# Kernel optimization log

Hardware: AMD Instinct MI355X
Metric: run time of the kernel (lower is better)

Reference implementation:

```python
import jax, jax.numpy as jnp
import numpy as np

GRAN = 4      # mask_spatial_granularity
STRIDE = 1    # dilate_stride
PAD = 1       # ExpandMask padding -> 3x3 all-ones dilation kernel


def setup_inputs() -> dict:
    key = jax.random.key(0)
    k1, k2, k3 = jax.random.split(key, 3)
    B, C, H, W = 32, 64, 112, 112
    G = 4
    mh, mw = H // STRIDE // GRAN, W // STRIDE // GRAN
    x = jax.random.normal(k1, (B, C, H, W), jnp.float32)
    weight = jax.random.normal(k2, (2 * G, C), jnp.float32) * 0.05  # 1x1 conv
    bias = jnp.zeros((2 * G,), jnp.float32).at[:G].set(5.0).at[G + 1:].set(1.0)
    # standard gumbel(0,1) noise for gumbel_softmax
    u = jax.random.uniform(k3, (B, 2, G, mh, mw), jnp.float32, 1e-10, 1.0)
    gumbel = -jnp.log(-jnp.log(u))
    temperature = jnp.float32(1.0)
    return {"x": x, "weight": weight, "bias": bias, "gumbel": gumbel,
            "temperature": temperature}


def reference(x, weight, bias, gumbel, temperature):
    B, C, H, W = x.shape
    G = weight.shape[0] // 2
    mh, mw = H // STRIDE // GRAN, W // STRIDE // GRAN   # mask grid (28,28)
    fh, fw = H // STRIDE, W // STRIDE                   # feature size (112,112)

    # adaptive_avg_pool2d (H,W evenly divisible by mask grid)
    m = x.reshape(B, C, mh, H // mh, mw, W // mw).mean(axis=(3, 5))
    flops = C * mh * mw
    # 1x1 conv
    m = jnp.einsum('bchw,oc->bohw', m, weight) + bias[None, :, None, None]
    flops += (weight.shape[0] * weight.shape[1] + weight.shape[1]) * mh * mw

    # gumbel_softmax over dim=1 with hard=True (straight-through)
    logits = m.reshape(B, 2, G, mh, mw)
    y_soft = jax.nn.softmax((logits + gumbel) / temperature, axis=1)
    idx = jnp.argmax(y_soft, axis=1)
    y_hard = jax.nn.one_hot(idx, 2, axis=1, dtype=y_soft.dtype)
    y = y_hard - jax.lax.stop_gradient(y_soft) + y_soft
    mask = y[:, 0]                                      # [B,G,mh,mw]
    sparsity = mask.sum() / mask.size

    # F.interpolate(size=feature_size), default mode='nearest' with integer factor
    mask = jnp.repeat(jnp.repeat(mask, fh // mh, axis=2), fw // mw, axis=3)

    # ExpandMask (stride=1): 3x3 all-ones full (cross-channel) conv, then >0.5
    dk = jnp.ones((G, G, 1 + 2 * PAD, 1 + 2 * PAD), mask.dtype)
    dil = jax.lax.conv_general_dilated(
        mask, dk, window_strides=(1, 1), padding=((PAD, PAD), (PAD, PAD)),
        dimension_numbers=('NCHW', 'OIHW', 'NCHW'))
    mask_dil = dil > 0.5
    sparsity_dil = jnp.mean(mask_dil.astype(jnp.float32))

    return mask, mask_dil, sparsity, sparsity_dil, flops
```

## Files before the change

kernel.cpp:

```cpp
#include <hip/hip_runtime.h>

#define MH 28
#define MW 28
#define CC 64
#define GG 4
#define NB 32
#define RPB 2

typedef float vf4 __attribute__((ext_vector_type(4)));

__device__ __forceinline__ int xcd_swz896(int phys) {
    return (phys & 7) * 112 + (phys >> 3);
}
__device__ __forceinline__ int xcd_swz448(int phys) {
    return (phys & 7) * 56 + (phys >> 3);
}


__global__ __launch_bounds__(256, 3) void masker_d1(
    const float* __restrict__ x, const float* __restrict__ w,
    const float* __restrict__ bias, const float* __restrict__ gum,
    unsigned char* __restrict__ coarse, unsigned char* __restrict__ anyb)
{
    const int blk = xcd_swz448(blockIdx.x);
    const int b = blk / 14, rp = blk - (blk / 14) * 14;
    const int chA = 2 * rp, chB = 2 * rp + 1;
    const int t = threadIdx.x;

    __shared__ float pooled[RPB][CC][MW];
    __shared__ float wlds[8 * CC];
    __shared__ float logits[RPB][8][MW];
    __shared__ unsigned char mlds[RPB][GG][MW];

    float g0a = 0.f, g1a = 0.f, g0b = 0.f, g1b = 0.f, bo = 0.f;
    if (t < GG * MW) {
        int g = t / MW, cw = t - g * MW;
        g0a = gum[((((size_t)b * 2 + 0) * GG + g) * MH + chA) * MW + cw];
        g1a = gum[((((size_t)b * 2 + 1) * GG + g) * MH + chA) * MW + cw];
        g0b = gum[((((size_t)b * 2 + 0) * GG + g) * MH + chB) * MW + cw];
        g1b = gum[((((size_t)b * 2 + 1) * GG + g) * MH + chB) * MW + cw];
    }
    if (t < 8 * MW) bo = bias[t / MW];
    if (t < 128) ((float4*)wlds)[t] = ((const float4*)w)[t];

    const float* xb = x + (size_t)b * CC * 12544 + (size_t)(8 * rp) * 112;
    #pragma unroll
    for (int r = 0; r < RPB; ++r) {
        vf4 rr[7][4];
        #pragma unroll
        for (int k = 0; k < 7; ++k) {
            int p  = t + 256 * k;
            int c  = p / MW;
            int cw = p - c * MW;
            const vf4* base = (const vf4*)(xb + (size_t)c * 12544
                                              + (size_t)(4 * r) * 112 + 4 * cw);
            #pragma unroll
            for (int hh = 0; hh < 4; ++hh)
                rr[k][hh] = __builtin_nontemporal_load(base + hh * 28);
        }
        #pragma unroll
        for (int k = 0; k < 7; ++k) {
            int p  = t + 256 * k;
            int c  = p / MW;
            int cw = p - c * MW;
            float s = 0.f;
            #pragma unroll
            for (int hh = 0; hh < 4; ++hh)
                s += rr[k][hh].x + rr[k][hh].y + rr[k][hh].z + rr[k][hh].w;
            pooled[r][c][cw] = s * 0.0625f;
        }
    }
    __syncthreads();

    if (t < 8 * MW) {
        int o = t / MW, cw = t - o * MW;
        float accA = bo, accB = bo;
        #pragma unroll
        for (int c = 0; c < CC; ++c) {
            float wv = wlds[o * CC + c];
            accA += pooled[0][c][cw] * wv;
            accB += pooled[1][c][cw] * wv;
        }
        logits[0][o][cw] = accA;
        logits[1][o][cw] = accB;
    }
    __syncthreads();

    if (t < GG * MW) {
        int g = t / MW, cw = t - g * MW;
        unsigned char mvA = (logits[0][g][cw] + g0a >= logits[0][g + 4][cw] + g1a) ? 1u : 0u;
        unsigned char mvB = (logits[1][g][cw] + g0b >= logits[1][g + 4][cw] + g1b) ? 1u : 0u;
        mlds[0][g][cw] = mvA;
        mlds[1][g][cw] = mvB;
        coarse[(((size_t)b * GG + g) * MH + chA) * MW + cw] = mvA;
        coarse[(((size_t)b * GG + g) * MH + chB) * MW + cw] = mvB;
    }
    __syncthreads();
    if (t < 2 * MW) {
        int r = t / MW, cw = t - r * MW;
        unsigned char a = mlds[r][0][cw] | mlds[r][1][cw] | mlds[r][2][cw] | mlds[r][3][cw];
        anyb[((size_t)b * MH + (2 * rp + r)) * MW + cw] = a;
    }
}

__global__ __launch_bounds__(256) void masker_d2(
    const unsigned char* __restrict__ coarse,
    const unsigned char* __restrict__ anyb,
    float* __restrict__ out_mask, float* __restrict__ out_dil,
    uint2* __restrict__ slots)
{
    const int blk = xcd_swz896(blockIdx.x);
    int b = blk / MH, ch = blk - (blk / MH) * MH, t = threadIdx.x;
    __shared__ float carr[GG][MW];
    __shared__ float R[3][MW + 2];
    __shared__ unsigned int sm[4], sd[4];

    unsigned int local_m = 0;
    if (t < GG * MW) {
        int g = t / MW, cw = t - g * MW;
        unsigned char mv = coarse[(((size_t)b * GG + g) * MH + ch) * MW + cw];
        carr[g][cw] = (float)mv;
        local_m = mv;
    }
    if (t < MW) {
        float a  = (float)anyb[((size_t)b * MH + ch) * MW + t];
        float am = (ch > 0)      ? (float)anyb[((size_t)b * MH + ch - 1) * MW + t] : 0.f;
        float ap = (ch < MH - 1) ? (float)anyb[((size_t)b * MH + ch + 1) * MW + t] : 0.f;
        R[0][t + 1] = fmaxf(a, am);
        R[1][t + 1] = a;
        R[2][t + 1] = fmaxf(a, ap);
    }
    if (t < 3) { R[t][0] = 0.f; R[t][MW + 1] = 0.f; }
    __syncthreads();

    unsigned int local_d = 0;
    #pragma unroll
    for (int k = 0; k < 7; ++k) {
        int idx = t + 256 * k;
        int g   = idx / 448;
        int rem = idx - g * 448;
        int hh  = rem / 112;
        int wfi = rem - hh * 112;
        int cw  = wfi >> 2;
        int wm  = wfi & 3;
        int rv  = (hh == 0) ? 0 : (hh == 3 ? 2 : 1);
        float d;
        if (wm == 0)      d = fmaxf(R[rv][cw],     R[rv][cw + 1]);
        else if (wm == 3) d = fmaxf(R[rv][cw + 1], R[rv][cw + 2]);
        else              d = R[rv][cw + 1];
        float mv = carr[g][cw];
        size_t o = (((size_t)b * GG + g) * 112 + (4 * ch + hh)) * 112 + wfi;
        __builtin_nontemporal_store(mv, &out_mask[o]);
        __builtin_nontemporal_store(d,  &out_dil[o]);
        local_d += (d > 0.5f) ? 1u : 0u;
    }

    #pragma unroll
    for (int off = 32; off; off >>= 1) {
        local_m += __shfl_down(local_m, off);
        local_d += __shfl_down(local_d, off);
    }
    if ((t & 63) == 0) { sm[t >> 6] = local_m; sd[t >> 6] = local_d; }
    __syncthreads();
    if (t == 0) {
        uint2 v;
        v.x = sm[0] + sm[1] + sm[2] + sm[3];
        v.y = sd[0] + sd[1] + sd[2] + sd[3];
        slots[blk] = v;
    }
}

__global__ __launch_bounds__(256) void masker_d3(
    const uint2* __restrict__ slots, float* __restrict__ out_scalars)
{
    int t = threadIdx.x;
    unsigned int m = 0, d = 0;
    for (int i = t; i < NB * MH; i += 256) { uint2 v = slots[i]; m += v.x; d += v.y; }
    #pragma unroll
    for (int off = 32; off; off >>= 1) {
        m += __shfl_down(m, off);
        d += __shfl_down(d, off);
    }
    __shared__ unsigned int sm[4], sd[4];
    if ((t & 63) == 0) { sm[t >> 6] = m; sd[t >> 6] = d; }
    __syncthreads();
    if (t == 0) {
        out_scalars[0] = (float)(sm[0] + sm[1] + sm[2] + sm[3]) / 100352.0f;
        out_scalars[1] = (float)(sd[0] + sd[1] + sd[2] + sd[3]) / 1605632.0f;
        out_scalars[2] = 501760.0f;
    }
}

extern "C" void kernel_launch(void* const* d_in, const int* in_sizes, int n_in,
                              void* d_out, int out_size, void* d_ws, size_t ws_size,
                              hipStream_t stream) {
    const float* x    = (const float*)d_in[0];
    const float* w    = (const float*)d_in[1];
    const float* bias = (const float*)d_in[2];
    const float* gum  = (const float*)d_in[3];

    float* out = (float*)d_out;
    const size_t n_mask = (size_t)NB * GG * 112 * 112;

    uint2*         slots  = (uint2*)d_ws;
    unsigned char* coarse = (unsigned char*)d_ws + 8192;
    unsigned char* anyb   = (unsigned char*)d_ws + 8192 + 100352;

    masker_d1<<<dim3(NB * MH / RPB), 256, 0, stream>>>(x, w, bias, gum, coarse, anyb);
    masker_d2<<<dim3(NB * MH), 256, 0, stream>>>(coarse, anyb, out, out + n_mask, slots);
    masker_d3<<<1, 256, 0, stream>>>(slots, out + 2 * n_mask);
}
```

Baseline: 28.00 us.

## Load contiguous channel slabs and pool via LDS row sums

The pooling phase now loads each channel's contiguous 8-row slab with consecutive threads covering consecutive float4s, instead of strided per-pooling-window loads. Each float4 is reduced to a row sum in a 28 KB shared buffer, and a second pass combines four row sums per pooled cell. The goal is fully coalesced global reads with more loads in flight per thread (28 float4). The cost is higher register pressure, more LDS use (which may reduce occupancy under launch_bounds 3) and extra barriers.

```diff
diff --git a/kernel.cpp b/kernel.cpp
--- a/kernel.cpp
+++ b/kernel.cpp
@@ -9,12 +9,8 @@
 
 typedef float vf4 __attribute__((ext_vector_type(4)));
 
-__device__ __forceinline__ int xcd_swz896(int phys) {
-    return (phys & 7) * 112 + (phys >> 3);
-}
-__device__ __forceinline__ int xcd_swz448(int phys) {
-    return (phys & 7) * 56 + (phys >> 3);
-}
+__device__ __forceinline__ int xcd_swz896(int phys) { return (phys & 7) * 112 + (phys >> 3); }
+__device__ __forceinline__ int xcd_swz448(int phys) { return (phys & 7) * 56  + (phys >> 3); }
 
 
 __global__ __launch_bounds__(256, 3) void masker_d1(
@@ -27,6 +23,7 @@
     const int chA = 2 * rp, chB = 2 * rp + 1;
     const int t = threadIdx.x;
 
+    __shared__ float rowsum[32 * 8 * MW];
     __shared__ float pooled[RPB][CC][MW];
     __shared__ float wlds[8 * CC];
     __shared__ float logits[RPB][8][MW];
@@ -44,33 +41,37 @@
     if (t < 128) ((float4*)wlds)[t] = ((const float4*)w)[t];
 
     const float* xb = x + (size_t)b * CC * 12544 + (size_t)(8 * rp) * 112;
-    #pragma unroll
-    for (int r = 0; r < RPB; ++r) {
-        vf4 rr[7][4];
+
+    #pragma unroll
+    for (int h = 0; h < 2; ++h) {
+        vf4 r[28];
+        #pragma unroll
+        for (int j = 0; j < 28; ++j) {
+            int f = t + 256 * j;
+            int s = f / 224;
+            int off = f - s * 224;
+            r[j] = __builtin_nontemporal_load(
+                (const vf4*)(xb + (size_t)(h * 32 + s) * 12544) + off);
+        }
+        #pragma unroll
+        for (int j = 0; j < 28; ++j) {
+            int f = t + 256 * j;
+            rowsum[f] = r[j].x + r[j].y + r[j].z + r[j].w;
+        }
+        __syncthreads();
         #pragma unroll
         for (int k = 0; k < 7; ++k) {
-            int p  = t + 256 * k;
-            int c  = p / MW;
-            int cw = p - c * MW;
-            const vf4* base = (const vf4*)(xb + (size_t)c * 12544
-                                              + (size_t)(4 * r) * 112 + 4 * cw);
-            #pragma unroll
-            for (int hh = 0; hh < 4; ++hh)
-                rr[k][hh] = __builtin_nontemporal_load(base + hh * 28);
-        }
-        #pragma unroll
-        for (int k = 0; k < 7; ++k) {
-            int p  = t + 256 * k;
-            int c  = p / MW;
-            int cw = p - c * MW;
-            float s = 0.f;
-            #pragma unroll
-            for (int hh = 0; hh < 4; ++hh)
-                s += rr[k][hh].x + rr[k][hh].y + rr[k][hh].z + rr[k][hh].w;
-            pooled[r][c][cw] = s * 0.0625f;
-        }
-    }
-    __syncthreads();
+            int idx = t + 256 * k;
+            int c_l = idx / 56;
+            int rem = idx - c_l * 56;
+            int rr  = rem / MW;
+            int cw  = rem - rr * MW;
+            const float* rs = &rowsum[c_l * 224 + rr * 4 * MW + cw];
+            pooled[rr][h * 32 + c_l][cw] =
+                (rs[0] + rs[MW] + rs[2 * MW] + rs[3 * MW]) * 0.0625f;
+        }
+        __syncthreads();
+    }
 
     if (t < 8 * MW) {
         int o = t / MW, cw = t - o * MW;
```

Result: no change. 27.66 us (-1.2%).
